# Optimization experiments

Hardware: AMD Instinct MI355X
Metric: run time of the kernel (lower is better)

The kernel has to match this reference:

```python
import jax, jax.numpy as jnp
import numpy as np

N = 131072      # nodes
E = 2097152     # edges (avg degree 16)
G = 64          # graphs in batch
D_IN = 64       # input node feature dim
D_E = 2         # raw edge feature dim
H = 128         # hidden dim
OUT = 128       # output dim
L = 3           # num GCN layers
GDIM = 6        # global feature dim
GP = H // 4     # global proj dim = 32
EPS = 1e-5      # BatchNorm eps


def setup_inputs() -> dict:
    key = jax.random.key(0)
    ks = jax.random.split(key, 24)
    s = lambda d: 1.0 / np.sqrt(d)
    return {
        "x": jax.random.normal(ks[0], (N, D_IN), jnp.float32),
        "edge_attr_raw": jax.random.normal(ks[1], (E, D_E), jnp.float32),
        "global_x": jax.random.normal(ks[2], (G, GDIM), jnp.float32),
        "W_in": jax.random.normal(ks[3], (D_IN, H), jnp.float32) * s(D_IN),
        "b_in": jnp.zeros((H,), jnp.float32),
        "W_edge": jax.random.normal(ks[4], (D_E, H), jnp.float32) * s(D_E),
        "b_edge": jnp.zeros((H,), jnp.float32),
        "W_gcn": jax.random.normal(ks[5], (L, H, H), jnp.float32) * s(H),
        "b_gcn": jnp.zeros((L, H), jnp.float32),
        "bn_gamma": jnp.ones((L, H), jnp.float32),
        "bn_beta": jnp.zeros((L, H), jnp.float32),
        "bn_mean": jax.random.normal(ks[6], (L, H), jnp.float32) * 0.1,
        "bn_var": jnp.ones((L, H), jnp.float32) + 0.1 * jax.random.uniform(ks[7], (L, H), jnp.float32),
        "W_gproj": jax.random.normal(ks[8], (GDIM, GP), jnp.float32) * s(GDIM),
        "b_gproj": jnp.zeros((GP,), jnp.float32),
        "W_gcomb": jax.random.normal(ks[9], (H + GP, OUT), jnp.float32) * s(H + GP),
        "b_gcomb": jnp.zeros((OUT,), jnp.float32),
        "row": jax.random.randint(ks[10], (E,), 0, N, jnp.int32),
        "col": jax.random.randint(ks[11], (E,), 0, N, jnp.int32),
        "batch": jnp.sort(jax.random.randint(ks[12], (N,), 0, G, jnp.int32)),
    }


def reference(x, edge_attr_raw, global_x, W_in, b_in, W_edge, b_edge,
              W_gcn, b_gcn, bn_gamma, bn_beta, bn_mean, bn_var,
              W_gproj, b_gproj, W_gcomb, b_gcomb, row, col, batch):
    n = x.shape[0]
    h = x @ W_in + b_in                                   # [N,H]
    ea = edge_attr_raw @ W_edge + b_edge                  # [E,H]
    ones_e = jnp.ones((row.shape[0],), h.dtype)
    deg = jnp.clip(jax.ops.segment_sum(ones_e, row, num_segments=n), 1.0)[:, None]
    for i in range(L):
        msg = h[col] * ea                                 # gather + edge weight [E,H]
        agg = jax.ops.segment_sum(msg, row, num_segments=n) / deg  # scatter-add + norm
        h = h + agg
        h = h @ W_gcn[i] + b_gcn[i]
        # eval-mode BatchNorm (running stats); dropout is identity in eval
        h = (h - bn_mean[i]) * (bn_gamma[i] / jnp.sqrt(bn_var[i] + EPS)) + bn_beta[i]
        h = jax.nn.relu(h)
    # global mean pool per graph
    gsum = jax.ops.segment_sum(h, batch, num_segments=G)
    gcnt = jnp.clip(jax.ops.segment_sum(jnp.ones((n,), h.dtype), batch, num_segments=G), 1.0)[:, None]
    g = gsum / gcnt                                       # [G,H]
    gp = jax.nn.relu(global_x @ W_gproj + b_gproj)        # [G,H//4]
    return jnp.concatenate([g, gp], axis=1) @ W_gcomb + b_gcomb  # [G,OUT]
```

## Files before the change

kernel.cpp:

```cpp
#include <hip/hip_runtime.h>
#include <stdint.h>

#define N_NODES 131072
#define N_EDGES 2097152
#define NG 64
#define HD 128
#define NL 3
#define EPSB 1e-5f

#define BUCKETS 256
#define BSHIFT 9
#define ROWS_PB 512
#define CHUNK 8192
#define NCHUNK (N_EDGES / CHUNK)
#define PAD_SLACK (7 * ROWS_PB)
#define CSR_CAP (N_EDGES + BUCKETS * (PAD_SLACK + 8))
#define TPAD 68

typedef unsigned short ushort_t;
typedef __bf16 bf16x8 __attribute__((ext_vector_type(8)));
typedef float f32x4 __attribute__((ext_vector_type(4)));

__device__ __forceinline__ float bf2f(uint32_t u16) {
    union { uint32_t i; float f; } c; c.i = u16 << 16; return c.f;
}
__device__ __forceinline__ float lo2f(uint32_t u) {
    union { uint32_t i; float f; } c; c.i = u << 16; return c.f;
}
__device__ __forceinline__ float hi2f(uint32_t u) {
    union { uint32_t i; float f; } c; c.i = u & 0xffff0000u; return c.f;
}
__device__ __forceinline__ ushort_t f2bf(float f) {
    union { float f; uint32_t i; } c; c.f = f;
    uint32_t u = c.i;
    uint32_t r = (u + 0x7fffu + ((u >> 16) & 1u)) >> 16;
    return (ushort_t)r;
}
__device__ __forceinline__ float ldf(const void* p, int i, int isb) {
    return isb ? bf2f(((const ushort_t*)p)[i]) : ((const float*)p)[i];
}

__global__ void detect_k(const uint32_t* __restrict__ ea, int* __restrict__ flag) {
    __shared__ int sm[256];
    int t = threadIdx.x;
    int plaus = 0;
    for (int j = 0; j < 16; j++) {
        uint32_t w = ea[t * 16 + j];
        uint32_t e0 = (w >> 7) & 0xFF;
        uint32_t e1 = (w >> 23) & 0xFF;
        plaus += (e0 >= 100 && e0 <= 140) ? 1 : 0;
        plaus += (e1 >= 100 && e1 <= 140) ? 1 : 0;
    }
    sm[t] = plaus;
    __syncthreads();
    for (int o = 128; o > 0; o >>= 1) {
        if (t < o) sm[t] += sm[t + o];
        __syncthreads();
    }
    if (t == 0) flag[0] = (sm[0] * 10 >= 8192 * 9) ? 1 : 0;
}

__global__ void prep_bn(const void* gamma, const void* beta,
                        const void* mean, const void* var,
                        const void* bgcn, float* sc, float* sh,
                        const int* __restrict__ flag) {
    int isb = flag[0];
    int i = blockIdx.x * 128 + threadIdx.x;
    if (i < NL * HD) {
        float g = ldf(gamma, i, isb), b = ldf(beta, i, isb);
        float m = ldf(mean, i, isb), v = ldf(var, i, isb), bb = ldf(bgcn, i, isb);
        float s = g / sqrtf(v + EPSB);
        sc[i] = s;
        sh[i] = (bb - m) * s + b;
    }
}

__global__ void transpose_k(const void* __restrict__ W, ushort_t* __restrict__ WTg,
                            const int* __restrict__ flag) {
    int isb = flag[0];
    int idx = blockIdx.x * 256 + threadIdx.x;
    if (idx < NL * HD * HD) {
        int l = idx >> 14;
        int rem = idx & 16383;
        int k = rem >> 7, n = rem & 127;
        WTg[l * 16384 + n * 128 + k] = f2bf(ldf(W, idx, isb));
    }
}

__global__ __launch_bounds__(256) void bucketA_k(
    const int* __restrict__ row, const int* __restrict__ col,
    const void* __restrict__ ea_raw,
    uint2* __restrict__ staged, uint32_t* __restrict__ cntmat,
    uint32_t* __restrict__ offmat, const int* __restrict__ flag)
{
    __shared__ int hist[256], offs[256], offs_ex[256], cur[256];
    int isb = flag[0];
    int t = threadIdx.x;
    int base = blockIdx.x * CHUNK;
    hist[t] = 0;
    __syncthreads();
#pragma unroll 4
    for (int j = 0; j < 32; j++) {
        int r = row[base + j * 256 + t];
        atomicAdd(&hist[r >> BSHIFT], 1);
    }
    __syncthreads();
    int v = hist[t];
    offs[t] = v;
    __syncthreads();
    for (int o = 1; o < 256; o <<= 1) {
        int u = (t >= o) ? offs[t - o] : 0;
        __syncthreads();
        offs[t] += u;
        __syncthreads();
    }
    offs_ex[t] = offs[t] - v;
    cur[t] = 0;
    cntmat[blockIdx.x * 256 + t] = (uint32_t)v;
    offmat[blockIdx.x * 256 + t] = (uint32_t)(offs[t] - v);
    __syncthreads();
    uint2* slice = staged + (size_t)blockIdx.x * CHUNK;
    for (int j = 0; j < 32; j++) {
        int e = base + j * 256 + t;
        int r = row[e];
        int b = r >> BSHIFT;
        uint32_t packed;
        if (isb) {
            packed = ((const uint32_t*)ea_raw)[e];
        } else {
            const float* f = (const float*)ea_raw + (size_t)e * 2;
            packed = (uint32_t)f2bf(f[0]) | ((uint32_t)f2bf(f[1]) << 16);
        }
        int pos = offs_ex[b] + atomicAdd(&cur[b], 1);
        slice[pos] = make_uint2((uint32_t)(((r & (ROWS_PB - 1)) << 17) | col[e]), packed);
    }
}

__global__ __launch_bounds__(256) void bucketsum_k(const uint32_t* __restrict__ cntmat,
                                                   uint32_t* __restrict__ btot) {
    __shared__ int sm[256];
    int b = blockIdx.x, t = threadIdx.x;
    sm[t] = (int)cntmat[t * 256 + b];
    __syncthreads();
    for (int o = 128; o > 0; o >>= 1) {
        if (t < o) sm[t] += sm[t + o];
        __syncthreads();
    }
    if (t == 0) btot[b] = (uint32_t)sm[0];
}

__global__ __launch_bounds__(256) void scan2_k(const uint32_t* __restrict__ btot,
                                               uint32_t* __restrict__ bbase) {
    __shared__ int sm[256];
    int t = threadIdx.x;
    int v = ((int)btot[t] + PAD_SLACK + 7) & ~7;
    sm[t] = v;
    __syncthreads();
    for (int o = 1; o < 256; o <<= 1) {
        int u = (t >= o) ? sm[t - o] : 0;
        __syncthreads();
        sm[t] += u;
        __syncthreads();
    }
    bbase[t] = (uint32_t)(sm[t] - v);
}

__global__ __launch_bounds__(512) void buildB_k(
    const uint2* __restrict__ staged, const uint32_t* __restrict__ cntmat,
    const uint32_t* __restrict__ offmat, const uint32_t* __restrict__ bbase,
    uint2* __restrict__ csr, int* __restrict__ csr_off, int* __restrict__ deg)
{
    __shared__ int runoff[257];
    __shared__ int runstart[256];
    __shared__ int hist2[512];
    __shared__ int po[512];
    __shared__ int cur2[512];
    int b = blockIdx.x, t = threadIdx.x;

    int myc = 0;
    if (t < 256) {
        myc = (int)cntmat[t * 256 + b];
        runstart[t] = t * CHUNK + (int)offmat[t * 256 + b];
        runoff[t] = myc;
    }
    __syncthreads();
    for (int o = 1; o < 256; o <<= 1) {
        int u = 0;
        if (t < 256 && t >= o) u = runoff[t - o];
        __syncthreads();
        if (t < 256) runoff[t] += u;
        __syncthreads();
    }
    if (t < 256) {
        int incl = runoff[t];
        runoff[t] = incl - myc;
        if (t == 255) runoff[256] = incl;
    }
    hist2[t] = 0;
    cur2[t] = 0;
    __syncthreads();
    int T = runoff[256];

    for (int i = t; i < T; i += 512) {
        int lo = 0, hi = 255;
        while (lo < hi) { int mid = (lo + hi + 1) >> 1; if (runoff[mid] <= i) lo = mid; else hi = mid - 1; }
        uint32_t x = staged[runstart[lo] + (i - runoff[lo])].x;
        atomicAdd(&hist2[x >> 17], 1);
    }
    __syncthreads();

    int pv = (hist2[t] + 7) & ~7;
    po[t] = pv;
    __syncthreads();
    for (int o = 1; o < 512; o <<= 1) {
        int u = (t >= o) ? po[t - o] : 0;
        __syncthreads();
        po[t] += u;
        __syncthreads();
    }
    po[t] -= pv;
    __syncthreads();

    int gbase = (int)bbase[b];
    csr_off[b * ROWS_PB + t] = gbase + po[t];
    deg[b * ROWS_PB + t] = hist2[t];

    for (int i = t; i < T; i += 512) {
        int lo = 0, hi = 255;
        while (lo < hi) { int mid = (lo + hi + 1) >> 1; if (runoff[mid] <= i) lo = mid; else hi = mid - 1; }
        uint2 en = staged[runstart[lo] + (i - runoff[lo])];
        int r = en.x >> 17;
        int pos = po[r] + atomicAdd(&cur2[r], 1);
        csr[gbase + pos] = make_uint2(en.x & 0x1FFFFu, en.y);
    }
    __syncthreads();
    int d = hist2[t], p = (d + 7) & ~7;
    for (int k = d; k < p; k++) csr[gbase + po[t] + k] = make_uint2(N_NODES, 0u);
}

__global__ __launch_bounds__(128, 6) void layer_fused_k(
    const uint32_t* __restrict__ h32,
    const int* __restrict__ csr_off, const int* __restrict__ degv,
    const uint2* __restrict__ csr,
    const void* __restrict__ Wedge, const void* __restrict__ bedge,
    const ushort_t* __restrict__ WTg,
    const float* __restrict__ sc, const float* __restrict__ sh,
    ushort_t* __restrict__ Hout,
    const int* __restrict__ flag)
{
    __shared__ uint32_t tile[16 * TPAD];
    int isb = flag[0];
    int tid = threadIdx.x;
    int wave = tid >> 6, lane = tid & 63;
    int quad = lane >> 4, l16 = lane & 15;
    int blockbase = blockIdx.x * 16;
    int nodebase = blockbase + wave * 8;

    float w0x = ldf(Wedge, 2 * lane, isb),       w0y = ldf(Wedge, 2 * lane + 1, isb);
    float w1x = ldf(Wedge, 128 + 2 * lane, isb), w1y = ldf(Wedge, 128 + 2 * lane + 1, isb);
    float bex = ldf(bedge, 2 * lane, isb),       bey = ldf(bedge, 2 * lane + 1, isb);

    int dg = degv[nodebase];
    int st = csr_off[nodebase];
    for (int i = 0; i < 8; i++) {
        int dgn = 0, stn = 0;
        if (i < 7) {
            dgn = degv[nodebase + i + 1];
            stn = csr_off[nodebase + i + 1];
        }
        uint32_t hn = h32[(uint32_t)(nodebase + i) * 64 + lane];

        int nit = (dg + 7) >> 3;
        const uint4* gp = (const uint4*)csr + (st >> 1);
        float ax = 0.f, ay = 0.f;
        for (int it = 0; it < nit; it++) {
            uint4 q0 = gp[0], q1 = gp[1], q2 = gp[2], q3 = gp[3];
            gp += 4;
            uint32_t cols[8] = {q0.x, q0.z, q1.x, q1.z, q2.x, q2.z, q3.x, q3.z};
            uint32_t eav[8]  = {q0.y, q0.w, q1.y, q1.w, q2.y, q2.w, q3.y, q3.w};
            uint32_t hv[8];
#pragma unroll
            for (int j = 0; j < 8; j++) hv[j] = h32[cols[j] * 64 + lane];
#pragma unroll
            for (int j = 0; j < 8; j++) {
                float a0 = bf2f(eav[j] & 0xffffu);
                float a1 = bf2f(eav[j] >> 16);
                float ex = fmaf(a1, w1x, fmaf(a0, w0x, bex));
                float ey = fmaf(a1, w1y, fmaf(a0, w0y, bey));
                ax = fmaf(lo2f(hv[j]), ex, ax);
                ay = fmaf(hi2f(hv[j]), ey, ay);
            }
        }
        float inv = 1.0f / (float)(dg > 0 ? dg : 1);
        float tx = lo2f(hn) + ax * inv;
        float ty = hi2f(hn) + ay * inv;
        tile[(wave * 8 + i) * TPAD + lane] = (uint32_t)f2bf(tx) | ((uint32_t)f2bf(ty) << 16);
        dg = dgn; st = stn;
    }
    __syncthreads();

    f32x4 acc[4];
#pragma unroll
    for (int c = 0; c < 4; c++) acc[c] = (f32x4){0.f, 0.f, 0.f, 0.f};

#pragma unroll
    for (int kk = 0; kk < 4; kk++) {
        bf16x8 a = *(const bf16x8*)(tile + l16 * TPAD + kk * 16 + quad * 4);
#pragma unroll
        for (int c = 0; c < 4; c++) {
            int gcol = wave * 64 + c * 16 + l16;
            bf16x8 b = *(const bf16x8*)(WTg + gcol * 128 + kk * 32 + quad * 8);
            acc[c] = __builtin_amdgcn_mfma_f32_16x16x32_bf16(a, b, acc[c], 0, 0, 0);
        }
    }
#pragma unroll
    for (int c = 0; c < 4; c++) {
        int gcol = wave * 64 + c * 16 + l16;
        float s = sc[gcol], o = sh[gcol];
#pragma unroll
        for (int r = 0; r < 4; r++) {
            float v = fmaxf(fmaf(acc[c][r], s, o), 0.f);
            Hout[(size_t)(blockbase + quad * 4 + r) * 128 + gcol] = f2bf(v);
        }
    }
}

__global__ __launch_bounds__(256) void gemm_in_k(
    const void* __restrict__ X, const void* __restrict__ W,
    const void* __restrict__ bin, ushort_t* __restrict__ Hout,
    const int* __restrict__ flag)
{
    __shared__ ushort_t WT[128 * 72];
    int isb = flag[0];
    int tid = threadIdx.x;
    for (int idx = tid; idx < 64 * 128; idx += 256) {
        int k = idx >> 7, n = idx & 127;
        WT[n * 72 + k] = f2bf(ldf(W, idx, isb));
    }
    __syncthreads();
    int wave = tid >> 6, lane = tid & 63;
    int quad = lane >> 4, l16 = lane & 15;
    int row = blockIdx.x * 64 + wave * 16 + l16;

    f32x4 acc[8];
#pragma unroll
    for (int c = 0; c < 8; c++) acc[c] = (f32x4){0.f, 0.f, 0.f, 0.f};

#pragma unroll
    for (int kk = 0; kk < 2; kk++) {
        int aoff = row * 64 + kk * 32 + quad * 8;
        union { bf16x8 v; ushort_t s[8]; } a;
        if (isb) {
            a.v = *(const bf16x8*)((const ushort_t*)X + aoff);
        } else {
            const float* xf = (const float*)X + aoff;
            f32x4 p0 = *(const f32x4*)xf;
            f32x4 p1 = *(const f32x4*)(xf + 4);
#pragma unroll
            for (int j = 0; j < 4; j++) { a.s[j] = f2bf(p0[j]); a.s[4 + j] = f2bf(p1[j]); }
        }
#pragma unroll
        for (int c = 0; c < 8; c++) {
            bf16x8 b = *(const bf16x8*)(&WT[(c * 16 + l16) * 72 + kk * 32 + quad * 8]);
            acc[c] = __builtin_amdgcn_mfma_f32_16x16x32_bf16(a.v, b, acc[c], 0, 0, 0);
        }
    }
    int rbase = blockIdx.x * 64 + wave * 16 + quad * 4;
#pragma unroll
    for (int c = 0; c < 8; c++) {
        int gcol = c * 16 + l16;
        float bb = ldf(bin, gcol, isb);
#pragma unroll
        for (int r = 0; r < 4; r++) {
            Hout[(rbase + r) * 128 + gcol] = f2bf(acc[c][r] + bb);
        }
    }
}

__global__ __launch_bounds__(128) void pool_k(
    const ushort_t* __restrict__ Hf, const int* __restrict__ batch,
    float* __restrict__ gsum, int* __restrict__ gcnt)
{
    int t = threadIdx.x;
    int n0 = blockIdx.x * 256;
    int n1 = n0 + 256;
    int cur = batch[n0];
    float s = 0.f; int c = 0;
    for (int n = n0; n < n1; n++) {
        int g = batch[n];
        if (g != cur) {
            atomicAdd(&gsum[cur * 128 + t], s);
            if (t == 0) atomicAdd(&gcnt[cur], c);
            s = 0.f; c = 0; cur = g;
        }
        s += bf2f(Hf[n * 128 + t]);
        c++;
    }
    atomicAdd(&gsum[cur * 128 + t], s);
    if (t == 0) atomicAdd(&gcnt[cur], c);
}

__global__ __launch_bounds__(128) void final_k(
    const float* __restrict__ gsum, const int* __restrict__ gcnt,
    const void* __restrict__ gx, const void* __restrict__ Wgp,
    const void* __restrict__ bgp, const void* __restrict__ Wgc,
    const void* __restrict__ bgc, void* __restrict__ out,
    const int* __restrict__ flag)
{
    __shared__ float gm[160];
    int isb = flag[0];
    int g = blockIdx.x, t = threadIdx.x;
    int c = gcnt[g]; if (c < 1) c = 1;
    gm[t] = gsum[g * 128 + t] / (float)c;
    if (t < 32) {
        float a = ldf(bgp, t, isb);
        for (int d = 0; d < 6; d++) a += ldf(gx, g * 6 + d, isb) * ldf(Wgp, d * 32 + t, isb);
        gm[128 + t] = fmaxf(a, 0.f);
    }
    __syncthreads();
    float a = ldf(bgc, t, isb);
    for (int k = 0; k < 160; k++) a += gm[k] * ldf(Wgc, k * 128 + t, isb);
    if (isb) ((ushort_t*)out)[g * 128 + t] = f2bf(a);
    else     ((float*)out)[g * 128 + t] = a;
}

extern "C" void kernel_launch(void* const* d_in, const int* in_sizes, int n_in,
                              void* d_out, int out_size, void* d_ws, size_t ws_size,
                              hipStream_t stream) {
    const void* x       = d_in[0];
    const void* ea_raw  = d_in[1];
    const void* gx      = d_in[2];
    const void* W_in    = d_in[3];
    const void* b_in    = d_in[4];
    const void* W_edge  = d_in[5];
    const void* b_edge  = d_in[6];
    const void* W_gcn   = d_in[7];
    const void* b_gcn   = d_in[8];
    const void* bn_g    = d_in[9];
    const void* bn_b    = d_in[10];
    const void* bn_m    = d_in[11];
    const void* bn_v    = d_in[12];
    const void* W_gproj = d_in[13];
    const void* b_gproj = d_in[14];
    const void* W_gcomb = d_in[15];
    const void* b_gcomb = d_in[16];
    const int* row   = (const int*)d_in[17];
    const int* col   = (const int*)d_in[18];
    const int* batch = (const int*)d_in[19];

    char* ws = (char*)d_ws;
    size_t off = 0;
    float*    gsum    = (float*)(ws + off);    off += (size_t)NG * HD * 4;
    int*      gcnt    = (int*)(ws + off);      off += 256;
    size_t zero_bytes = off;
    int*      flag    = (int*)(ws + off);      off += 256;
    uint32_t* cntmat  = (uint32_t*)(ws + off); off += 256 * 256 * 4;
    uint32_t* offmat  = (uint32_t*)(ws + off); off += 256 * 256 * 4;
    uint32_t* btot    = (uint32_t*)(ws + off); off += 1024;
    uint32_t* bbase   = (uint32_t*)(ws + off); off += 1024;
    int*      csr_off = (int*)(ws + off);      off += (size_t)N_NODES * 4;
    int*      deg     = (int*)(ws + off);      off += (size_t)N_NODES * 4;
    ushort_t* wtg     = (ushort_t*)(ws + off); off += (size_t)NL * HD * HD * 2;
    float*    sc      = (float*)(ws + off);    off += (size_t)NL * HD * 4;
    float*    sh      = (float*)(ws + off);    off += (size_t)NL * HD * 4;
    uint2*    csr     = (uint2*)(ws + off);    off += (size_t)CSR_CAP * 8;
    ushort_t* hA      = (ushort_t*)(ws + off); off += (size_t)(N_NODES + 1) * HD * 2;
    ushort_t* hB      = (ushort_t*)(ws + off); off += (size_t)(N_NODES + 1) * HD * 2;
    uint2*    staged  = (uint2*)hB;

    hipMemsetAsync(ws, 0, zero_bytes, stream);
    hipMemsetAsync(hA + (size_t)N_NODES * HD, 0, HD * 2, stream);
    hipMemsetAsync(hB + (size_t)N_NODES * HD, 0, HD * 2, stream);
    detect_k<<<1, 256, 0, stream>>>((const uint32_t*)ea_raw, flag);
    prep_bn<<<3, 128, 0, stream>>>(bn_g, bn_b, bn_m, bn_v, b_gcn, sc, sh, flag);
    transpose_k<<<(NL * HD * HD + 255) / 256, 256, 0, stream>>>(W_gcn, wtg, flag);

    bucketA_k<<<NCHUNK, 256, 0, stream>>>(row, col, ea_raw, staged, cntmat, offmat, flag);
    bucketsum_k<<<BUCKETS, 256, 0, stream>>>(cntmat, btot);
    scan2_k<<<1, 256, 0, stream>>>(btot, bbase);
    buildB_k<<<BUCKETS, 512, 0, stream>>>(staged, cntmat, offmat, bbase, csr, csr_off, deg);

    gemm_in_k<<<N_NODES / 64, 256, 0, stream>>>(x, W_in, b_in, hA, flag);

    ushort_t* hin = hA;
    ushort_t* hout = hB;
    for (int l = 0; l < NL; l++) {
        layer_fused_k<<<N_NODES / 16, 128, 0, stream>>>(
            (const uint32_t*)hin, csr_off, deg, csr,
            W_edge, b_edge, wtg + (size_t)l * HD * HD, sc + l * HD, sh + l * HD,
            hout, flag);
        ushort_t* tmp = hin; hin = hout; hout = tmp;
    }

    pool_k<<<N_NODES / 256, 128, 0, stream>>>(hin, batch, gsum, gcnt);
    final_k<<<NG, 128, 0, stream>>>(gsum, gcnt, gx, W_gproj, b_gproj,
                                    W_gcomb, b_gcomb, d_out, flag);
}
```

Before: 681.0 us.

## Split each wave into two half-waves gathering alternate edges with 8-byte loads

The edge aggregation now has each half-wave handle alternating edges of a node. Each lane loads 8 bytes (4 bf16 features) per neighbour instead of 4 bytes. The loop processes 16 edges per iteration with 8 gathers in flight, and a tail handles the last group of 8. The two half-wave partial sums are combined with a cross-lane shuffle before the tile write. This is meant to raise memory-level parallelism and use wider gather loads, at the cost of more registers for edge weights and accumulators and an extra shuffle reduction.

```diff
diff --git a/kernel.cpp b/kernel.cpp
--- a/kernel.cpp
+++ b/kernel.cpp
@@ -237,6 +237,20 @@
     int d = hist2[t], p = (d + 7) & ~7;
     for (int k = d; k < p; k++) csr[gbase + po[t] + k] = make_uint2(N_NODES, 0u);
 }
+
+#define SLOT(m, gv)                                                  \
+    {                                                                \
+        float a0 = bf2f((m).y & 0xffffu);                            \
+        float a1 = bf2f((m).y >> 16);                                \
+        float e0 = fmaf(a1, w1f0, fmaf(a0, w0f0, bef0));             \
+        float e1 = fmaf(a1, w1f1, fmaf(a0, w0f1, bef1));             \
+        float e2 = fmaf(a1, w1f2, fmaf(a0, w0f2, bef2));             \
+        float e3 = fmaf(a1, w1f3, fmaf(a0, w0f3, bef3));             \
+        acc0 = fmaf(lo2f((gv).x), e0, acc0);                         \
+        acc1 = fmaf(hi2f((gv).x), e1, acc1);                         \
+        acc2 = fmaf(lo2f((gv).y), e2, acc2);                         \
+        acc3 = fmaf(hi2f((gv).y), e3, acc3);                         \
+    }
 
 __global__ __launch_bounds__(128, 6) void layer_fused_k(
     const uint32_t* __restrict__ h32,
@@ -253,12 +267,16 @@
     int tid = threadIdx.x;
     int wave = tid >> 6, lane = tid & 63;
     int quad = lane >> 4, l16 = lane & 15;
+    int half = lane >> 5, c32 = lane & 31;
     int blockbase = blockIdx.x * 16;
     int nodebase = blockbase + wave * 8;
 
-    float w0x = ldf(Wedge, 2 * lane, isb),       w0y = ldf(Wedge, 2 * lane + 1, isb);
-    float w1x = ldf(Wedge, 128 + 2 * lane, isb), w1y = ldf(Wedge, 128 + 2 * lane + 1, isb);
-    float bex = ldf(bedge, 2 * lane, isb),       bey = ldf(bedge, 2 * lane + 1, isb);
+    float w0f0 = ldf(Wedge, 4 * c32 + 0, isb), w0f1 = ldf(Wedge, 4 * c32 + 1, isb);
+    float w0f2 = ldf(Wedge, 4 * c32 + 2, isb), w0f3 = ldf(Wedge, 4 * c32 + 3, isb);
+    float w1f0 = ldf(Wedge, 128 + 4 * c32 + 0, isb), w1f1 = ldf(Wedge, 128 + 4 * c32 + 1, isb);
+    float w1f2 = ldf(Wedge, 128 + 4 * c32 + 2, isb), w1f3 = ldf(Wedge, 128 + 4 * c32 + 3, isb);
+    float bef0 = ldf(bedge, 4 * c32 + 0, isb), bef1 = ldf(bedge, 4 * c32 + 1, isb);
+    float bef2 = ldf(bedge, 4 * c32 + 2, isb), bef3 = ldf(bedge, 4 * c32 + 3, isb);
 
     int dg = degv[nodebase];
     int st = csr_off[nodebase];
@@ -268,33 +286,50 @@
             dgn = degv[nodebase + i + 1];
             stn = csr_off[nodebase + i + 1];
         }
-        uint32_t hn = h32[(uint32_t)(nodebase + i) * 64 + lane];
-
-        int nit = (dg + 7) >> 3;
-        const uint4* gp = (const uint4*)csr + (st >> 1);
-        float ax = 0.f, ay = 0.f;
-        for (int it = 0; it < nit; it++) {
-            uint4 q0 = gp[0], q1 = gp[1], q2 = gp[2], q3 = gp[3];
-            gp += 4;
-            uint32_t cols[8] = {q0.x, q0.z, q1.x, q1.z, q2.x, q2.z, q3.x, q3.z};
-            uint32_t eav[8]  = {q0.y, q0.w, q1.y, q1.w, q2.y, q2.w, q3.y, q3.w};
-            uint32_t hv[8];
-#pragma unroll
-            for (int j = 0; j < 8; j++) hv[j] = h32[cols[j] * 64 + lane];
-#pragma unroll
-            for (int j = 0; j < 8; j++) {
-                float a0 = bf2f(eav[j] & 0xffffu);
-                float a1 = bf2f(eav[j] >> 16);
-                float ex = fmaf(a1, w1x, fmaf(a0, w0x, bex));
-                float ey = fmaf(a1, w1y, fmaf(a0, w0y, bey));
-                ax = fmaf(lo2f(hv[j]), ex, ax);
-                ay = fmaf(hi2f(hv[j]), ey, ay);
-            }
-        }
+        uint2 hn = *(const uint2*)&h32[(uint32_t)(nodebase + i) * 64 + c32 * 2];
+
+        int ngrp = (dg + 7) >> 3;
+        const uint2* ep = csr + st;
+        float acc0 = 0.f, acc1 = 0.f, acc2 = 0.f, acc3 = 0.f;
+        int g = 0;
+        for (; g + 2 <= ngrp; g += 2) {
+            uint2 m0 = ep[0 + half],  m1 = ep[2 + half],  m2 = ep[4 + half],  m3 = ep[6 + half];
+            uint2 m4 = ep[8 + half],  m5 = ep[10 + half], m6 = ep[12 + half], m7 = ep[14 + half];
+            ep += 16;
+            uint2 g0 = *(const uint2*)&h32[m0.x * 64 + c32 * 2];
+            uint2 g1 = *(const uint2*)&h32[m1.x * 64 + c32 * 2];
+            uint2 g2 = *(const uint2*)&h32[m2.x * 64 + c32 * 2];
+            uint2 g3 = *(const uint2*)&h32[m3.x * 64 + c32 * 2];
+            uint2 g4 = *(const uint2*)&h32[m4.x * 64 + c32 * 2];
+            uint2 g5 = *(const uint2*)&h32[m5.x * 64 + c32 * 2];
+            uint2 g6 = *(const uint2*)&h32[m6.x * 64 + c32 * 2];
+            uint2 g7 = *(const uint2*)&h32[m7.x * 64 + c32 * 2];
+            SLOT(m0, g0); SLOT(m1, g1); SLOT(m2, g2); SLOT(m3, g3);
+            SLOT(m4, g4); SLOT(m5, g5); SLOT(m6, g6); SLOT(m7, g7);
+        }
+        if (g < ngrp) {
+            uint2 m0 = ep[0 + half], m1 = ep[2 + half], m2 = ep[4 + half], m3 = ep[6 + half];
+            uint2 g0 = *(const uint2*)&h32[m0.x * 64 + c32 * 2];
+            uint2 g1 = *(const uint2*)&h32[m1.x * 64 + c32 * 2];
+            uint2 g2 = *(const uint2*)&h32[m2.x * 64 + c32 * 2];
+            uint2 g3 = *(const uint2*)&h32[m3.x * 64 + c32 * 2];
+            SLOT(m0, g0); SLOT(m1, g1); SLOT(m2, g2); SLOT(m3, g3);
+        }
+        acc0 += __shfl_xor(acc0, 32);
+        acc1 += __shfl_xor(acc1, 32);
+        acc2 += __shfl_xor(acc2, 32);
+        acc3 += __shfl_xor(acc3, 32);
+
         float inv = 1.0f / (float)(dg > 0 ? dg : 1);
-        float tx = lo2f(hn) + ax * inv;
-        float ty = hi2f(hn) + ay * inv;
-        tile[(wave * 8 + i) * TPAD + lane] = (uint32_t)f2bf(tx) | ((uint32_t)f2bf(ty) << 16);
+        float t0 = lo2f(hn.x) + acc0 * inv;
+        float t1 = hi2f(hn.x) + acc1 * inv;
+        float t2 = lo2f(hn.y) + acc2 * inv;
+        float t3 = hi2f(hn.y) + acc3 * inv;
+        if (half == 0) {
+            uint32_t p0 = (uint32_t)f2bf(t0) | ((uint32_t)f2bf(t1) << 16);
+            uint32_t p1 = (uint32_t)f2bf(t2) | ((uint32_t)f2bf(t3) << 16);
+            *(uint2*)&tile[(wave * 8 + i) * TPAD + c32 * 2] = make_uint2(p0, p1);
+        }
         dg = dgn; st = stn;
     }
     __syncthreads();
```

Measured after the change: 730.1 us. +7.2%, slower.
